# Optimization experiments

Hardware: AMD Instinct MI355X
Metric: run time of the kernel (lower is better)

The kernel has to match this reference:

```python
import jax, jax.numpy as jnp
import numpy as np

H, N_EMB, D_EMB, D_UP = 1024, 8192, 512, 2048
B, T, BB, M, K_LABELS = 4, 4096, 512, 4096, 64


def _rms(x, w, eps=1e-6):
    xf = x.astype(jnp.float32)
    var = jnp.mean(xf * xf, axis=-1, keepdims=True)
    return (w * (xf * jax.lax.rsqrt(var + eps))).astype(x.dtype)


def setup_inputs() -> dict:
    key = jax.random.key(0)
    ks = jax.random.split(key, 8)
    bt = B * T
    inp = jax.random.normal(ks[0], (B, T, H), jnp.float32)
    w_k = jax.random.normal(ks[1], (N_EMB, H), jnp.float32) * 0.02
    w_v = jax.random.normal(ks[2], (N_EMB, D_EMB), jnp.float32) * 0.02
    w_up = jax.random.normal(ks[3], (D_UP, D_EMB), jnp.float32) * 0.02
    w_mix = jax.random.normal(ks[4], (H, D_UP + H), jnp.float32) * 0.02
    fw = jax.random.permutation(ks[5], bt)
    bw = jnp.argsort(fw)  # inverse permutation
    seq_sort = jax.random.randint(ks[6], (bt,), 0, K_LABELS)
    keep_cols = jnp.arange(M)  # keep first M of N_EMB rows
    emb_alloc = jnp.arange(N_EMB) % K_LABELS  # every label present among kept rows
    starts = jnp.zeros((bt,), jnp.int32)
    ends = jnp.full((bt,), M, jnp.int32)
    return {
        'input': inp, 'fw': fw, 'bw': bw, 'seq_sort': seq_sort,
        'keep_cols': keep_cols, 'emb_alloc': emb_alloc,
        'starts': starts, 'ends': ends, 'bb': BB,
        'w_k_weight': w_k, 'w_v_weight': w_v, 'w_up_weight': w_up,
        'w_mix_weight': w_mix,
        'norm_in_weight': jnp.ones((H,), jnp.float32),
        'norm_out_weight': jnp.ones((D_UP,), jnp.float32),
    }


def reference(input, fw, bw, seq_sort, keep_cols, emb_alloc, starts, ends, bb,
              w_k_weight, w_v_weight, w_up_weight, w_mix_weight,
              norm_in_weight, norm_out_weight):
    b, t, h = input.shape
    A = _rms(input, norm_in_weight)                      # [b,t,h]
    Bm = w_k_weight[keep_cols]                           # [m,h]
    Cm = w_v_weight[keep_cols]                           # [m,d_emb]
    la = emb_alloc[keep_cols]                            # [m]
    A = A.reshape(-1, h)[fw].reshape(-1, bb, h)          # [nb,bb,h]
    ss = seq_sort.reshape(-1, bb)                        # [nb,bb]
    st = starts.reshape(-1, bb).min(axis=-1)             # [nb]
    en = ends.reshape(-1, bb).max(axis=-1)               # [nb]
    # ragged per-block slice B[start:end] expressed as a kv range mask,
    # combined with the equality mask seq_sort[q] == emb_alloc[kv]
    scores = jnp.einsum('nqh,kh->nqk', A, Bm)            # [nb,bb,m]
    kv = jnp.arange(Bm.shape[0])
    mask = ((ss[:, :, None] == la[None, None, :])
            & (kv[None, None, :] >= st[:, None, None])
            & (kv[None, None, :] < en[:, None, None]))
    scores = jnp.where(mask, scores, -jnp.inf)
    p = jax.nn.softmax(scores, axis=-1)
    comb = jnp.einsum('nqk,kd->nqd', p, Cm)              # [nb,bb,d_emb]
    d_emb = Cm.shape[-1]
    comb = comb.reshape(-1, d_emb)[bw].reshape(b, t, d_emb)
    up = comb @ w_up_weight.T                            # [b,t,d_up]
    cat = jnp.concatenate([_rms(up, norm_out_weight), input], axis=-1)
    return cat @ w_mix_weight.T                          # [b,t,h]
```

## Files before the change

### kernel.cpp

```cpp
#include <hip/hip_runtime.h>
#include <hip/hip_bf16.h>
#include <cstdint>
#include <cstddef>

#define Hh 1024
#define D_EMB 512
#define D_UP 2048
#define BT 16384
#define BB_ 512
#define Mm 4096
#define MmP 4160
#define NB 32
#define KL 64
#define NXCD 8

typedef __attribute__((ext_vector_type(4))) float f4;
typedef __attribute__((ext_vector_type(4))) __bf16 bf4;
typedef __attribute__((ext_vector_type(8))) __bf16 bf8;
typedef __attribute__((ext_vector_type(4))) float f32x4;

__device__ __forceinline__ void gl_lds16(const void* g, void* l) {
  __builtin_amdgcn_global_load_lds((__attribute__((address_space(1))) void*)g,
                                   (__attribute__((address_space(3))) void*)l, 16, 0, 0);
}

__global__ __launch_bounds__(256) void conv_bf16_kernel(const float* __restrict__ src,
                                                        __bf16* __restrict__ dst, int n4) {
  int i = blockIdx.x * 256 + threadIdx.x;
  if (i >= n4) return;
  f4 v = ((const f4*)src)[i];
  bf4 o = {(__bf16)v[0], (__bf16)v[1], (__bf16)v[2], (__bf16)v[3]};
  ((bf4*)dst)[i] = o;
}

__global__ __launch_bounds__(256) void gather_bf16_kernel(const float* __restrict__ src,
                                                          const int* __restrict__ idx,
                                                          __bf16* __restrict__ dst, int cols4) {
  int row = blockIdx.x;
  const f4* s = (const f4*)src + (size_t)idx[row] * cols4;
  bf4* d = (bf4*)dst + (size_t)row * cols4;
  for (int i = threadIdx.x; i < cols4; i += 256) {
    f4 v = s[i];
    bf4 o = {(__bf16)v[0], (__bf16)v[1], (__bf16)v[2], (__bf16)v[3]};
    d[i] = o;
  }
}

__global__ __launch_bounds__(256) void la_kernel(const int* __restrict__ keep,
                                                 const int* __restrict__ emb,
                                                 int* __restrict__ la, int m) {
  int i = blockIdx.x * 256 + threadIdx.x;
  if (i < m) la[i] = emb[keep[i]];
}

__global__ __launch_bounds__(256) void range_kernel(const int* __restrict__ starts,
                                                    const int* __restrict__ ends,
                                                    int* __restrict__ stA, int* __restrict__ enA) {
  int n = blockIdx.x;
  int t = threadIdx.x, lane = t & 63, wv = t >> 6;
  int s1 = min(starts[n * BB_ + t], starts[n * BB_ + t + 256]);
  int e1 = max(ends[n * BB_ + t], ends[n * BB_ + t + 256]);
#pragma unroll
  for (int off = 32; off; off >>= 1) {
    s1 = min(s1, __shfl_xor(s1, off));
    e1 = max(e1, __shfl_xor(e1, off));
  }
  __shared__ int ssh[4], esh[4];
  if (lane == 0) { ssh[wv] = s1; esh[wv] = e1; }
  __syncthreads();
  if (t == 0) {
    int s = ssh[0], e = esh[0];
#pragma unroll
    for (int k = 1; k < 4; ++k) { s = min(s, ssh[k]); e = max(e, esh[k]); }
    stA[n] = s; enA[n] = e;
  }
}

__global__ __launch_bounds__(256) void hist_kernel(const int* __restrict__ la,
                                                   int* __restrict__ goff) {
  __shared__ int cnt[KL];
  int tid = threadIdx.x;
  if (tid < KL) cnt[tid] = 0;
  __syncthreads();
  for (int k = tid; k < Mm; k += 256) atomicAdd(&cnt[la[k]], 1);
  __syncthreads();
  if (tid == 0) {
    int a = 0;
    for (int s = 0; s < KL; ++s) { goff[s] = a; a += cnt[s]; }
    goff[KL] = a;
  }
}

__global__ __launch_bounds__(256) void place_kernel(const int* __restrict__ la,
                                                    const int* __restrict__ keep,
                                                    const int* __restrict__ goff,
                                                    int* __restrict__ gk,
                                                    int* __restrict__ ridx) {
  int s = blockIdx.x;
  int tid = threadIdx.x, lane = tid & 63, wv = tid >> 6;
  __shared__ int wc[4];
  __shared__ int run;
  if (tid == 0) run = goff[s];
  __syncthreads();
  for (int base = 0; base < Mm; base += 256) {
    int k = base + tid;
    bool f = (la[k] == s);
    unsigned long long msk = __ballot(f);
    int myidx = __popcll(msk & ((1ull << lane) - 1ull));
    if (lane == 0) wc[wv] = __popcll(msk);
    __syncthreads();
    int woff = 0, tot = 0;
#pragma unroll
    for (int w = 0; w < 4; ++w) {
      if (w < wv) woff += wc[w];
      tot += wc[w];
    }
    int rbase = run;
    if (f) {
      int p = rbase + woff + myidx;
      gk[p] = k;
      ridx[p] = keep[k];
    }
    __syncthreads();
    if (tid == 0) run = rbase + tot;
    __syncthreads();
  }
}

__global__ __launch_bounds__(256) void lohi_kernel(const int* __restrict__ gk,
                                                   const int* __restrict__ goff,
                                                   const int* __restrict__ stA,
                                                   const int* __restrict__ enA,
                                                   int* __restrict__ loA, int* __restrict__ hiA) {
  int i = blockIdx.x * 256 + threadIdx.x;
  if (i >= NB * KL) return;
  int n = i / KL, s = i % KL;
  int b = goff[s], e = goff[s + 1];
  int st = stA[n], en = enA[n];
  int lo = b, hi = e;
  while (lo < hi) { int mid = (lo + hi) >> 1; if (gk[mid] < st) lo = mid + 1; else hi = mid; }
  int L = lo;
  lo = b; hi = e;
  while (lo < hi) { int mid = (lo + hi) >> 1; if (gk[mid] < en) lo = mid + 1; else hi = mid; }
  loA[i] = L;
  hiA[i] = lo;
}

__global__ __launch_bounds__(256) void vt_kernel(const float* __restrict__ wv_,
                                                 const int* __restrict__ ridx,
                                                 __bf16* __restrict__ VT) {
  int pb = blockIdx.x * 64;
  int db = blockIdx.y * 64;
  __shared__ float T[64][65];
  int t = threadIdx.x;
  int dl = t & 63, g = t >> 6;
  for (int i = g * 16; i < g * 16 + 16; ++i) {
    int r = ridx[pb + i];
    T[dl][i] = wv_[(size_t)r * D_EMB + db + dl];
  }
  __syncthreads();
  int pl = t & 63;
  for (int j = g * 16; j < g * 16 + 16; ++j) {
    VT[(size_t)(db + j) * MmP + pb + pl] = (__bf16)T[j][pl];
  }
}

__global__ __launch_bounds__(256) void qsort_kernel(const int* __restrict__ seq_sort,
                                                    int* __restrict__ qidx,
                                                    int* __restrict__ qoffA,
                                                    int* __restrict__ qcntA) {
  int n = blockIdx.x, tid = threadIdx.x;
  __shared__ int cnt[KL], pos[KL], pref[KL];
  if (tid < KL) cnt[tid] = 0;
  __syncthreads();
  int s0 = seq_sort[n * BB_ + tid];
  int s1 = seq_sort[n * BB_ + tid + 256];
  atomicAdd(&cnt[s0], 1);
  atomicAdd(&cnt[s1], 1);
  __syncthreads();
  if (tid == 0) {
    int a = 0;
    for (int s = 0; s < KL; ++s) { pref[s] = a; a += cnt[s]; }
  }
  __syncthreads();
  if (tid < KL) {
    pos[tid] = pref[tid];
    qoffA[n * KL + tid] = pref[tid];
    qcntA[n * KL + tid] = cnt[tid];
  }
  __syncthreads();
  int p0 = atomicAdd(&pos[s0], 1);
  qidx[n * BB_ + p0] = n * BB_ + tid;
  int p1 = atomicAdd(&pos[s1], 1);
  qidx[n * BB_ + p1] = n * BB_ + tid + 256;
}

__global__ __launch_bounds__(256) void rms_in_kernel(const float* __restrict__ input,
                                                     const int* __restrict__ fw,
                                                     const float* __restrict__ wn,
                                                     __bf16* __restrict__ Aperm,
                                                     __bf16* __restrict__ inb) {
  int wv = threadIdx.x >> 6, lane = threadIdx.x & 63;
  int j = blockIdx.x * 4 + wv;
  {
    const f4* src = (const f4*)(input + (size_t)fw[j] * Hh);
    f4 v[4];
    float ss = 0.f;
#pragma unroll
    for (int c = 0; c < 4; ++c) {
      v[c] = src[c * 64 + lane];
      ss += v[c][0] * v[c][0] + v[c][1] * v[c][1] + v[c][2] * v[c][2] + v[c][3] * v[c][3];
    }
#pragma unroll
    for (int off = 32; off; off >>= 1) ss += __shfl_xor(ss, off);
    float sc = rsqrtf(ss * (1.f / Hh) + 1e-6f);
    const f4* w4 = (const f4*)wn;
    bf4* dst = (bf4*)(Aperm + (size_t)j * Hh);
#pragma unroll
    for (int c = 0; c < 4; ++c) {
      f4 w = w4[c * 64 + lane];
      bf4 o = {(__bf16)(v[c][0] * sc * w[0]), (__bf16)(v[c][1] * sc * w[1]),
               (__bf16)(v[c][2] * sc * w[2]), (__bf16)(v[c][3] * sc * w[3])};
      dst[c * 64 + lane] = o;
    }
  }
  {
    const f4* src = (const f4*)(input + (size_t)j * Hh);
    bf4* dst = (bf4*)(inb + (size_t)j * Hh);
#pragma unroll
    for (int c = 0; c < 4; ++c) {
      f4 t = src[c * 64 + lane];
      bf4 o = {(__bf16)t[0], (__bf16)t[1], (__bf16)t[2], (__bf16)t[3]};
      dst[c * 64 + lane] = o;
    }
  }
}

__global__ __launch_bounds__(256) void attn3_kernel(const __bf16* __restrict__ Aperm,
                                                    const __bf16* __restrict__ Ks,
                                                    const __bf16* __restrict__ VT,
                                                    const int* __restrict__ qidx,
                                                    const int* __restrict__ qoffA,
                                                    const int* __restrict__ qcntA,
                                                    const int* __restrict__ loA,
                                                    const int* __restrict__ hiA,
                                                    const int* __restrict__ fw,
                                                    __bf16* __restrict__ comb) {
  int g = blockIdx.x;
  int qcnt = qcntA[g];
  if (qcnt == 0) return;
  int n = g >> 6;
  int qbase = n * BB_ + qoffA[g];
  int lo = loA[g], hi = hiA[g];
  if (lo >= hi) return;
  int tid = threadIdx.x, lane = tid & 63, wv = tid >> 6;
  int c = lane & 15, rg = lane >> 4;
  __shared__ float Sbuf[16][66];
  __shared__ __align__(16) __bf16 Plds[16][72];
  __shared__ float scl[16], lrec[16];

  for (int qt = 0; qt < qcnt; qt += 16) {
    int ql = qt + c;
    int j = qidx[qbase + (ql < qcnt ? ql : 0)];
    const __bf16* arow = Aperm + (size_t)j * Hh + rg * 8;

    float m[4] = {-1e30f, -1e30f, -1e30f, -1e30f};
    float l[4] = {0.f, 0.f, 0.f, 0.f};
    f32x4 acc[8];
    f32x4 zero = {0.f, 0.f, 0.f, 0.f};
#pragma unroll
    for (int t8 = 0; t8 < 8; ++t8) acc[t8] = zero;

    for (int p0 = lo; p0 < hi; p0 += 64) {
      int kvcol = p0 + wv * 16 + c;
      const __bf16* brow = Ks + (size_t)kvcol * Hh + rg * 8;
      f32x4 sacc = zero;
#pragma unroll
      for (int ks = 0; ks < 32; ++ks) {
        bf8 af = *(const bf8*)(arow + ks * 32);
        bf8 bf_ = *(const bf8*)(brow + ks * 32);
        sacc = __builtin_amdgcn_mfma_f32_16x16x32_bf16(af, bf_, sacc, 0, 0, 0);
      }
      bool valid = kvcol < hi;
#pragma unroll
      for (int r = 0; r < 4; ++r) Sbuf[rg * 4 + r][wv * 16 + c] = valid ? sacc[r] : -1e30f;
      __syncthreads();

#pragma unroll
      for (int r = 0; r < 4; ++r) {
        int q = wv * 4 + r;
        float s = Sbuf[q][lane];
        float cm = s;
#pragma unroll
        for (int off = 32; off; off >>= 1) cm = fmaxf(cm, __shfl_xor(cm, off));
        float mn = fmaxf(m[r], cm);
        float sc = __expf(m[r] - mn);
        float pv = __expf(s - mn);
        float ssum = pv;
#pragma unroll
        for (int off = 32; off; off >>= 1) ssum += __shfl_xor(ssum, off);
        l[r] = l[r] * sc + ssum;
        m[r] = mn;
        Plds[q][lane] = (__bf16)pv;
        if (lane == 0) scl[q] = sc;
      }
      __syncthreads();

      float sf[4];
#pragma unroll
      for (int r = 0; r < 4; ++r) sf[r] = scl[rg * 4 + r];
#pragma unroll
      for (int t8 = 0; t8 < 8; ++t8)
#pragma unroll
        for (int r = 0; r < 4; ++r) acc[t8][r] *= sf[r];

      bf8 pa0 = *(const bf8*)(&Plds[c][rg * 8]);
      bf8 pa1 = *(const bf8*)(&Plds[c][32 + rg * 8]);
#pragma unroll
      for (int tt = 0; tt < 8; ++tt) {
        int d = wv * 128 + tt * 16 + c;
        const __bf16* vrow = VT + (size_t)d * MmP + p0 + rg * 8;
        bf8 b0 = *(const bf8*)(vrow);
        bf8 b1 = *(const bf8*)(vrow + 32);
        acc[tt] = __builtin_amdgcn_mfma_f32_16x16x32_bf16(pa0, b0, acc[tt], 0, 0, 0);
        acc[tt] = __builtin_amdgcn_mfma_f32_16x16x32_bf16(pa1, b1, acc[tt], 0, 0, 0);
      }
      __syncthreads();
    }

    if (lane == 0) {
#pragma unroll
      for (int r = 0; r < 4; ++r) lrec[wv * 4 + r] = l[r];
    }
    __syncthreads();
    float inv[4];
    size_t obase[4];
    bool oval[4];
#pragma unroll
    for (int r = 0; r < 4; ++r) {
      int qq = qt + rg * 4 + r;
      oval[r] = qq < qcnt;
      int j2 = qidx[qbase + (oval[r] ? qq : 0)];
      obase[r] = (size_t)fw[j2] * D_EMB;
      float lv = lrec[rg * 4 + r];
      inv[r] = 1.f / lv;
    }
#pragma unroll
    for (int tt = 0; tt < 8; ++tt) {
      int d = wv * 128 + tt * 16 + c;
#pragma unroll
      for (int r = 0; r < 4; ++r) {
        if (oval[r]) comb[obase[r] + d] = (__bf16)(acc[tt][r] * inv[r]);
      }
    }
    __syncthreads();
  }
}

template <bool OUT_BF16>
__global__ __launch_bounds__(512, 2) void gemm8p(const __bf16* __restrict__ x0, int k0,
                                                 const __bf16* __restrict__ x1, int k1,
                                                 const __bf16* __restrict__ w,
                                                 void* __restrict__ outp, int Mt, int Nt) {
  __shared__ __align__(16) __bf16 lds[4][2][256 * 32];
  const int nwg = Mt * Nt;
  const int bid = blockIdx.x;
  const int swz = (bid % NXCD) * (nwg / NXCD) + bid / NXCD;
  const int m0 = (swz / Nt) * 256, n0 = (swz % Nt) * 256;
  const int K = k0 + k1;
  const int NT = K >> 5;
  const int N = Nt * 256;
  const int tid = threadIdx.x, lane = tid & 63, wvi = tid >> 6;
  const int wr = wvi >> 2, wc = wvi & 3;

  const int srow = tid >> 2;
  const int spb = (tid & 3) * 16;

  const int c = lane & 15, rg = lane >> 4;
  const int fa_off = c * 64 + ((rg ^ ((c >> 1) & 3)) << 4);

  auto stage_half = [&](int t, int j) {
    int kg = t * 32;
    const __bf16* xs;
    int ld, kk;
    if (kg < k0) { xs = x0; ld = k0; kk = kg; }
    else         { xs = x1; ld = k1; kk = kg - k0; }
    int b = t & 3;
    int r = j * 128 + srow;
    int lcol = (spb ^ (((r >> 1) & 3) << 4)) >> 1;
    gl_lds16(xs + (size_t)(m0 + r) * ld + kk + lcol,
             (void*)((char*)&lds[b][0][0] + r * 64 + spb));
    gl_lds16(w + (size_t)(n0 + r) * K + kg + lcol,
             (void*)((char*)&lds[b][1][0] + r * 64 + spb));
  };

  f32x4 acc[8][4];
  f32x4 zero = {0.f, 0.f, 0.f, 0.f};
#pragma unroll
  for (int a = 0; a < 8; ++a)
#pragma unroll
    for (int bnx = 0; bnx < 4; ++bnx) acc[a][bnx] = zero;

#pragma unroll
  for (int t = 0; t < 3; ++t) {
    stage_half(t, 0);
    stage_half(t, 1);
  }
  asm volatile("s_waitcnt vmcnt(8)" ::: "memory");
  __builtin_amdgcn_s_barrier();

  for (int t = 0; t < NT; ++t) {
    const char* Abase = (const char*)&lds[t & 3][0][0];
    const char* Bbase = (const char*)&lds[t & 3][1][0];
    bf8 bfr[4];
#pragma unroll
    for (int ri = 0; ri < 2; ++ri) {
      if (t + 3 < NT) stage_half(t + 3, ri);
      bf8 afr[4];
#pragma unroll
      for (int fi = 0; fi < 4; ++fi)
        afr[fi] = *(const bf8*)(Abase + (wr * 128 + ri * 64 + fi * 16) * 64 + fa_off);
      if (ri == 0) {
#pragma unroll
        for (int fi = 0; fi < 4; ++fi)
          bfr[fi] = *(const bf8*)(Bbase + (wc * 64 + fi * 16) * 64 + fa_off);
      }
      __builtin_amdgcn_s_barrier();
      __builtin_amdgcn_s_setprio(1);
#pragma unroll
      for (int fi = 0; fi < 4; ++fi)
#pragma unroll
        for (int ni = 0; ni < 4; ++ni)
          acc[ri * 4 + fi][ni] =
              __builtin_amdgcn_mfma_f32_16x16x32_bf16(afr[fi], bfr[ni], acc[ri * 4 + fi][ni], 0, 0, 0);
      __builtin_amdgcn_s_setprio(0);
      if (ri == 1) asm volatile("s_waitcnt vmcnt(8)" ::: "memory");
      __builtin_amdgcn_s_barrier();
    }
  }

  const int r0 = (lane >> 4) * 4, cc = lane & 15;
#pragma unroll
  for (int mi = 0; mi < 8; ++mi) {
    int rowb = m0 + wr * 128 + (mi >> 2) * 64 + (mi & 3) * 16 + r0;
#pragma unroll
    for (int ni = 0; ni < 4; ++ni) {
      int col = n0 + wc * 64 + ni * 16 + cc;
#pragma unroll
      for (int r = 0; r < 4; ++r) {
        float v = acc[mi][ni][r];
        if (OUT_BF16)
          ((__bf16*)outp)[(size_t)(rowb + r) * N + col] = (__bf16)v;
        else
          ((float*)outp)[(size_t)(rowb + r) * N + col] = v;
      }
    }
  }
}

__global__ __launch_bounds__(256) void rms_up_kernel(__bf16* __restrict__ up,
                                                     const float* __restrict__ wn) {
  int wv = threadIdx.x >> 6, lane = threadIdx.x & 63;
  size_t j = (size_t)blockIdx.x * 4 + wv;
  bf8* row = (bf8*)(up + j * D_UP);
  bf8 v[4];
  float ss = 0.f;
#pragma unroll
  for (int c = 0; c < 4; ++c) {
    v[c] = row[c * 64 + lane];
#pragma unroll
    for (int i = 0; i < 8; ++i) { float f = (float)v[c][i]; ss += f * f; }
  }
#pragma unroll
  for (int off = 32; off; off >>= 1) ss += __shfl_xor(ss, off);
  float sc = rsqrtf(ss * (1.f / D_UP) + 1e-6f);
#pragma unroll
  for (int c = 0; c < 4; ++c) {
    int ebase = (c * 64 + lane) * 8;
    f4 wa = *(const f4*)(wn + ebase);
    f4 wb = *(const f4*)(wn + ebase + 4);
    bf8 o;
#pragma unroll
    for (int i = 0; i < 4; ++i) o[i] = (__bf16)((float)v[c][i] * sc * wa[i]);
#pragma unroll
    for (int i = 0; i < 4; ++i) o[4 + i] = (__bf16)((float)v[c][4 + i] * sc * wb[i]);
    row[c * 64 + lane] = o;
  }
}

extern "C" void kernel_launch(void* const* d_in, const int* in_sizes, int n_in, void* d_out,
                              int out_size, void* d_ws, size_t ws_size, hipStream_t stream) {
  const float* input = (const float*)d_in[0];
  const int* fw = (const int*)d_in[1];
  const int* seq_sort = (const int*)d_in[3];
  const int* keep_cols = (const int*)d_in[4];
  const int* emb_alloc = (const int*)d_in[5];
  const int* starts = (const int*)d_in[6];
  const int* ends = (const int*)d_in[7];
  const float* w_k = (const float*)d_in[9];
  const float* w_v = (const float*)d_in[10];
  const float* w_up = (const float*)d_in[11];
  const float* w_mix = (const float*)d_in[12];
  const float* w_nin = (const float*)d_in[13];
  const float* w_nout = (const float*)d_in[14];

  char* p = (char*)d_ws;
  auto take = [&](size_t b) {
    void* r = (void*)p;
    p += (b + 255) & ~(size_t)255;
    return r;
  };
  __bf16* Aperm = (__bf16*)take((size_t)BT * Hh * 2);
  __bf16* inb = (__bf16*)take((size_t)BT * Hh * 2);
  __bf16* comb = (__bf16*)take((size_t)BT * D_EMB * 2);
  __bf16* up = (__bf16*)take((size_t)BT * D_UP * 2);
  __bf16* Ks = (__bf16*)take((size_t)MmP * Hh * 2);
  __bf16* VT = (__bf16*)take((size_t)D_EMB * MmP * 2);
  __bf16* wupB = (__bf16*)take((size_t)D_UP * D_EMB * 2);
  __bf16* wmixB = (__bf16*)take((size_t)Hh * (D_UP + Hh) * 2);
  int* la = (int*)take(Mm * 4);
  int* stA = (int*)take(NB * 4);
  int* enA = (int*)take(NB * 4);
  int* goff = (int*)take((KL + 1) * 4);
  int* gk = (int*)take(Mm * 4);
  int* ridx = (int*)take(Mm * 4);
  int* loA = (int*)take(NB * KL * 4);
  int* hiA = (int*)take(NB * KL * 4);
  int* qidx = (int*)take(BT * 4);
  int* qoffA = (int*)take(NB * KL * 4);
  int* qcntA = (int*)take(NB * KL * 4);

  conv_bf16_kernel<<<(D_UP * D_EMB / 4 + 255) / 256, 256, 0, stream>>>(w_up, wupB, D_UP * D_EMB / 4);
  conv_bf16_kernel<<<(Hh * (D_UP + Hh) / 4 + 255) / 256, 256, 0, stream>>>(w_mix, wmixB,
                                                                           Hh * (D_UP + Hh) / 4);
  la_kernel<<<Mm / 256, 256, 0, stream>>>(keep_cols, emb_alloc, la, Mm);
  range_kernel<<<NB, 256, 0, stream>>>(starts, ends, stA, enA);
  hist_kernel<<<1, 256, 0, stream>>>(la, goff);
  place_kernel<<<KL, 256, 0, stream>>>(la, keep_cols, goff, gk, ridx);
  lohi_kernel<<<(NB * KL + 255) / 256, 256, 0, stream>>>(gk, goff, stA, enA, loA, hiA);
  gather_bf16_kernel<<<Mm, 256, 0, stream>>>(w_k, ridx, Ks, Hh / 4);
  vt_kernel<<<dim3(Mm / 64, D_EMB / 64), 256, 0, stream>>>(w_v, ridx, VT);
  qsort_kernel<<<NB, 256, 0, stream>>>(seq_sort, qidx, qoffA, qcntA);

  rms_in_kernel<<<BT / 4, 256, 0, stream>>>(input, fw, w_nin, Aperm, inb);
  attn3_kernel<<<NB * KL, 256, 0, stream>>>(Aperm, Ks, VT, qidx, qoffA, qcntA, loA, hiA, fw, comb);
  gemm8p<true><<<BT / 256 * (D_UP / 256), 512, 0, stream>>>(comb, D_EMB, (const __bf16*)nullptr, 0,
                                                            wupB, (void*)up, BT / 256, D_UP / 256);
  rms_up_kernel<<<BT / 4, 256, 0, stream>>>(up, w_nout);
  gemm8p<false><<<BT / 256 * (Hh / 256), 512, 0, stream>>>(up, D_UP, inb, Hh, wmixB, d_out,
                                                           BT / 256, Hh / 256);
}
```

Measured before the change: 332.9 us.

## Restructure attention to one wave per group with register-resident softmax

The attention kernel now gives each wave its own (block,label) group instead of one workgroup per group. Each wave computes a 16x64 score tile with four MFMA chains, does the online softmax in registers via lane shuffles, and keeps all 512 output dims in 32 accumulators. This removes the LDS score/P buffers and three __syncthreads per kv tile, and stages output through LDS for coalesced 16-byte stores. The RMS-in kernel now reads input rows contiguously once and scatters Aperm through the inverse permutation. VT padding columns are zero-filled so the pad region is defined. The cost is heavy register use: 128 accumulator floats per lane, with launch bounds of 2 workgroups per CU. Load balance across waves may also be uneven because label groups differ in size.

```diff
diff --git a/kernel.cpp b/kernel.cpp
--- a/kernel.cpp
+++ b/kernel.cpp
@@ -155,8 +155,13 @@
   int t = threadIdx.x;
   int dl = t & 63, g = t >> 6;
   for (int i = g * 16; i < g * 16 + 16; ++i) {
-    int r = ridx[pb + i];
-    T[dl][i] = wv_[(size_t)r * D_EMB + db + dl];
+    int pos = pb + i;
+    float val = 0.f;
+    if (pos < Mm) {
+      int r = ridx[pos];
+      val = wv_[(size_t)r * D_EMB + db + dl];
+    }
+    T[dl][i] = val;
   }
   __syncthreads();
   int pl = t & 63;
@@ -196,164 +201,165 @@
 }
 
 __global__ __launch_bounds__(256) void rms_in_kernel(const float* __restrict__ input,
-                                                     const int* __restrict__ fw,
+                                                     const int* __restrict__ bw,
                                                      const float* __restrict__ wn,
                                                      __bf16* __restrict__ Aperm,
                                                      __bf16* __restrict__ inb) {
   int wv = threadIdx.x >> 6, lane = threadIdx.x & 63;
   int j = blockIdx.x * 4 + wv;
-  {
-    const f4* src = (const f4*)(input + (size_t)fw[j] * Hh);
-    f4 v[4];
-    float ss = 0.f;
-#pragma unroll
-    for (int c = 0; c < 4; ++c) {
-      v[c] = src[c * 64 + lane];
-      ss += v[c][0] * v[c][0] + v[c][1] * v[c][1] + v[c][2] * v[c][2] + v[c][3] * v[c][3];
-    }
-#pragma unroll
-    for (int off = 32; off; off >>= 1) ss += __shfl_xor(ss, off);
-    float sc = rsqrtf(ss * (1.f / Hh) + 1e-6f);
-    const f4* w4 = (const f4*)wn;
-    bf4* dst = (bf4*)(Aperm + (size_t)j * Hh);
-#pragma unroll
-    for (int c = 0; c < 4; ++c) {
-      f4 w = w4[c * 64 + lane];
-      bf4 o = {(__bf16)(v[c][0] * sc * w[0]), (__bf16)(v[c][1] * sc * w[1]),
-               (__bf16)(v[c][2] * sc * w[2]), (__bf16)(v[c][3] * sc * w[3])};
-      dst[c * 64 + lane] = o;
-    }
-  }
-  {
-    const f4* src = (const f4*)(input + (size_t)j * Hh);
-    bf4* dst = (bf4*)(inb + (size_t)j * Hh);
-#pragma unroll
-    for (int c = 0; c < 4; ++c) {
-      f4 t = src[c * 64 + lane];
-      bf4 o = {(__bf16)t[0], (__bf16)t[1], (__bf16)t[2], (__bf16)t[3]};
-      dst[c * 64 + lane] = o;
-    }
-  }
-}
-
-__global__ __launch_bounds__(256) void attn3_kernel(const __bf16* __restrict__ Aperm,
-                                                    const __bf16* __restrict__ Ks,
-                                                    const __bf16* __restrict__ VT,
-                                                    const int* __restrict__ qidx,
-                                                    const int* __restrict__ qoffA,
-                                                    const int* __restrict__ qcntA,
-                                                    const int* __restrict__ loA,
-                                                    const int* __restrict__ hiA,
-                                                    const int* __restrict__ fw,
-                                                    __bf16* __restrict__ comb) {
-  int g = blockIdx.x;
+  const f4* src = (const f4*)(input + (size_t)j * Hh);
+  f4 v[4];
+  float ss = 0.f;
+#pragma unroll
+  for (int c = 0; c < 4; ++c) {
+    v[c] = src[c * 64 + lane];
+    ss += v[c][0] * v[c][0] + v[c][1] * v[c][1] + v[c][2] * v[c][2] + v[c][3] * v[c][3];
+  }
+#pragma unroll
+  for (int off = 32; off; off >>= 1) ss += __shfl_xor(ss, off);
+  float sc = rsqrtf(ss * (1.f / Hh) + 1e-6f);
+  bf4* dstI = (bf4*)(inb + (size_t)j * Hh);
+#pragma unroll
+  for (int c = 0; c < 4; ++c) {
+    bf4 o = {(__bf16)v[c][0], (__bf16)v[c][1], (__bf16)v[c][2], (__bf16)v[c][3]};
+    dstI[c * 64 + lane] = o;
+  }
+  int dj = bw[j];
+  const f4* w4 = (const f4*)wn;
+  bf4* dstA = (bf4*)(Aperm + (size_t)dj * Hh);
+#pragma unroll
+  for (int c = 0; c < 4; ++c) {
+    f4 w = w4[c * 64 + lane];
+    bf4 o = {(__bf16)(v[c][0] * sc * w[0]), (__bf16)(v[c][1] * sc * w[1]),
+             (__bf16)(v[c][2] * sc * w[2]), (__bf16)(v[c][3] * sc * w[3])};
+    dstA[c * 64 + lane] = o;
+  }
+}
+
+__global__ __launch_bounds__(256, 2) void attn4_kernel(const __bf16* __restrict__ Aperm,
+                                                       const __bf16* __restrict__ Ks,
+                                                       const __bf16* __restrict__ VT,
+                                                       const int* __restrict__ qidx,
+                                                       const int* __restrict__ qoffA,
+                                                       const int* __restrict__ qcntA,
+                                                       const int* __restrict__ loA,
+                                                       const int* __restrict__ hiA,
+                                                       const int* __restrict__ fw,
+                                                       __bf16* __restrict__ comb) {
+  __shared__ __align__(16) __bf16 owb[4][16][528];
+  int wv = threadIdx.x >> 6, lane = threadIdx.x & 63;
+  int g = blockIdx.x * 4 + wv;
   int qcnt = qcntA[g];
-  if (qcnt == 0) return;
+  int lo = loA[g], hi = hiA[g];
+  if (qcnt == 0 || lo >= hi) return;
   int n = g >> 6;
   int qbase = n * BB_ + qoffA[g];
-  int lo = loA[g], hi = hiA[g];
-  if (lo >= hi) return;
-  int tid = threadIdx.x, lane = tid & 63, wv = tid >> 6;
   int c = lane & 15, rg = lane >> 4;
-  __shared__ float Sbuf[16][66];
-  __shared__ __align__(16) __bf16 Plds[16][72];
-  __shared__ float scl[16], lrec[16];
+  int sl_a = c + ((rg & 1) << 5);
+  int sl_b = sl_a + 16;
+  bool hiKt = (rg & 2) != 0;
+  const __bf16* vbase = VT + (size_t)c * MmP + rg * 8;
 
   for (int qt = 0; qt < qcnt; qt += 16) {
     int ql = qt + c;
-    int j = qidx[qbase + (ql < qcnt ? ql : 0)];
-    const __bf16* arow = Aperm + (size_t)j * Hh + rg * 8;
-
-    float m[4] = {-1e30f, -1e30f, -1e30f, -1e30f};
-    float l[4] = {0.f, 0.f, 0.f, 0.f};
-    f32x4 acc[8];
+    int j = qidx[qbase + (ql < qcnt ? ql : qcnt - 1)];
+    const __bf16* qrow = Aperm + (size_t)j * Hh + rg * 8;
+
+    float m = -1e30f, lsum = 0.f;
+    f32x4 acc[32];
     f32x4 zero = {0.f, 0.f, 0.f, 0.f};
 #pragma unroll
-    for (int t8 = 0; t8 < 8; ++t8) acc[t8] = zero;
+    for (int ff = 0; ff < 32; ++ff) acc[ff] = zero;
 
     for (int p0 = lo; p0 < hi; p0 += 64) {
-      int kvcol = p0 + wv * 16 + c;
-      const __bf16* brow = Ks + (size_t)kvcol * Hh + rg * 8;
-      f32x4 sacc = zero;
+      const __bf16* kb = Ks + (size_t)(p0 + c) * Hh + rg * 8;
+      f32x4 sN[4];
+#pragma unroll
+      for (int kt = 0; kt < 4; ++kt) sN[kt] = zero;
 #pragma unroll
       for (int ks = 0; ks < 32; ++ks) {
-        bf8 af = *(const bf8*)(arow + ks * 32);
-        bf8 bf_ = *(const bf8*)(brow + ks * 32);
-        sacc = __builtin_amdgcn_mfma_f32_16x16x32_bf16(af, bf_, sacc, 0, 0, 0);
+        bf8 qf = *(const bf8*)(qrow + ks * 32);
+#pragma unroll
+        for (int kt = 0; kt < 4; ++kt) {
+          bf8 kf = *(const bf8*)(kb + (size_t)kt * 16 * Hh + ks * 32);
+          sN[kt] = __builtin_amdgcn_mfma_f32_16x16x32_bf16(kf, qf, sN[kt], 0, 0, 0);
+        }
       }
-      bool valid = kvcol < hi;
-#pragma unroll
-      for (int r = 0; r < 4; ++r) Sbuf[rg * 4 + r][wv * 16 + c] = valid ? sacc[r] : -1e30f;
-      __syncthreads();
-
-#pragma unroll
-      for (int r = 0; r < 4; ++r) {
-        int q = wv * 4 + r;
-        float s = Sbuf[q][lane];
-        float cm = s;
-#pragma unroll
-        for (int off = 32; off; off >>= 1) cm = fmaxf(cm, __shfl_xor(cm, off));
-        float mn = fmaxf(m[r], cm);
-        float sc = __expf(m[r] - mn);
-        float pv = __expf(s - mn);
-        float ssum = pv;
-#pragma unroll
-        for (int off = 32; off; off >>= 1) ssum += __shfl_xor(ssum, off);
-        l[r] = l[r] * sc + ssum;
-        m[r] = mn;
-        Plds[q][lane] = (__bf16)pv;
-        if (lane == 0) scl[q] = sc;
+      float smax = -1e30f;
+#pragma unroll
+      for (int kt = 0; kt < 4; ++kt)
+#pragma unroll
+        for (int r = 0; r < 4; ++r) {
+          int kv = p0 + kt * 16 + rg * 4 + r;
+          float sv = (kv < hi) ? sN[kt][r] : -1e30f;
+          sN[kt][r] = sv;
+          smax = fmaxf(smax, sv);
+        }
+      smax = fmaxf(smax, __shfl_xor(smax, 16));
+      smax = fmaxf(smax, __shfl_xor(smax, 32));
+      float mn = fmaxf(m, smax);
+      float sc = __expf(m - mn);
+      float sum = 0.f;
+#pragma unroll
+      for (int kt = 0; kt < 4; ++kt)
+#pragma unroll
+        for (int r = 0; r < 4; ++r) {
+          float pv = __expf(sN[kt][r] - mn);
+          sN[kt][r] = pv;
+          sum += pv;
+        }
+      sum += __shfl_xor(sum, 16);
+      sum += __shfl_xor(sum, 32);
+      lsum = lsum * sc + sum;
+      m = mn;
+#pragma unroll
+      for (int ff = 0; ff < 32; ++ff) acc[ff] = acc[ff] * sc;
+
+      bf8 pbh[2];
+#pragma unroll
+      for (int h = 0; h < 2; ++h) {
+        float e[8];
+#pragma unroll
+        for (int r = 0; r < 4; ++r) {
+          float a0 = __shfl(sN[2 * h][r], sl_a);
+          float a1 = __shfl(sN[2 * h + 1][r], sl_a);
+          e[r] = hiKt ? a1 : a0;
+          float b0 = __shfl(sN[2 * h][r], sl_b);
+          float b1 = __shfl(sN[2 * h + 1][r], sl_b);
+          e[4 + r] = hiKt ? b1 : b0;
+        }
+        bf8 pb;
+#pragma unroll
+        for (int i = 0; i < 8; ++i) pb[i] = (__bf16)e[i];
+        pbh[h] = pb;
       }
-      __syncthreads();
-
-      float sf[4];
-#pragma unroll
-      for (int r = 0; r < 4; ++r) sf[r] = scl[rg * 4 + r];
-#pragma unroll
-      for (int t8 = 0; t8 < 8; ++t8)
-#pragma unroll
-        for (int r = 0; r < 4; ++r) acc[t8][r] *= sf[r];
-
-      bf8 pa0 = *(const bf8*)(&Plds[c][rg * 8]);
-      bf8 pa1 = *(const bf8*)(&Plds[c][32 + rg * 8]);
-#pragma unroll
-      for (int tt = 0; tt < 8; ++tt) {
-        int d = wv * 128 + tt * 16 + c;
-        const __bf16* vrow = VT + (size_t)d * MmP + p0 + rg * 8;
-        bf8 b0 = *(const bf8*)(vrow);
-        bf8 b1 = *(const bf8*)(vrow + 32);
-        acc[tt] = __builtin_amdgcn_mfma_f32_16x16x32_bf16(pa0, b0, acc[tt], 0, 0, 0);
-        acc[tt] = __builtin_amdgcn_mfma_f32_16x16x32_bf16(pa1, b1, acc[tt], 0, 0, 0);
+#pragma unroll
+      for (int ff = 0; ff < 32; ++ff) {
+        const __bf16* vr = vbase + (size_t)ff * (16 * MmP) + p0;
+        bf8 v0 = *(const bf8*)(vr);
+        bf8 v1 = *(const bf8*)(vr + 32);
+        acc[ff] = __builtin_amdgcn_mfma_f32_16x16x32_bf16(v0, pbh[0], acc[ff], 0, 0, 0);
+        acc[ff] = __builtin_amdgcn_mfma_f32_16x16x32_bf16(v1, pbh[1], acc[ff], 0, 0, 0);
       }
-      __syncthreads();
-    }
-
-    if (lane == 0) {
-#pragma unroll
-      for (int r = 0; r < 4; ++r) lrec[wv * 4 + r] = l[r];
-    }
-    __syncthreads();
-    float inv[4];
-    size_t obase[4];
-    bool oval[4];
-#pragma unroll
-    for (int r = 0; r < 4; ++r) {
-      int qq = qt + rg * 4 + r;
-      oval[r] = qq < qcnt;
-      int j2 = qidx[qbase + (oval[r] ? qq : 0)];
-      obase[r] = (size_t)fw[j2] * D_EMB;
-      float lv = lrec[rg * 4 + r];
-      inv[r] = 1.f / lv;
-    }
-#pragma unroll
-    for (int tt = 0; tt < 8; ++tt) {
-      int d = wv * 128 + tt * 16 + c;
-#pragma unroll
-      for (int r = 0; r < 4; ++r) {
-        if (oval[r]) comb[obase[r] + d] = (__bf16)(acc[tt][r] * inv[r]);
-      }
-    }
-    __syncthreads();
+    }
+
+    float inv = 1.f / lsum;
+#pragma unroll
+    for (int ff = 0; ff < 32; ++ff) {
+      bf4 o;
+#pragma unroll
+      for (int r = 0; r < 4; ++r) o[r] = (__bf16)(acc[ff][r] * inv);
+      *(bf4*)&owb[wv][c][ff * 16 + rg * 4] = o;
+    }
+    int qp = qt + (lane >> 2);
+    bool vq = qp < qcnt;
+    size_t ob = 0;
+    if (vq) ob = (size_t)fw[qidx[qbase + qp]] * D_EMB + (lane & 3) * 8;
+#pragma unroll
+    for (int it = 0; it < 16; ++it) {
+      bf8 o = *(const bf8*)&owb[wv][lane >> 2][(lane & 3) * 8 + it * 32];
+      if (vq) *(bf8*)(comb + ob + (size_t)it * 32) = o;
+    }
   }
 }
 
@@ -492,6 +498,7 @@
                               int out_size, void* d_ws, size_t ws_size, hipStream_t stream) {
   const float* input = (const float*)d_in[0];
   const int* fw = (const int*)d_in[1];
+  const int* bw = (const int*)d_in[2];
   const int* seq_sort = (const int*)d_in[3];
   const int* keep_cols = (const int*)d_in[4];
   const int* emb_alloc = (const int*)d_in[5];
@@ -539,11 +546,12 @@
   place_kernel<<<KL, 256, 0, stream>>>(la, keep_cols, goff, gk, ridx);
   lohi_kernel<<<(NB * KL + 255) / 256, 256, 0, stream>>>(gk, goff, stA, enA, loA, hiA);
   gather_bf16_kernel<<<Mm, 256, 0, stream>>>(w_k, ridx, Ks, Hh / 4);
-  vt_kernel<<<dim3(Mm / 64, D_EMB / 64), 256, 0, stream>>>(w_v, ridx, VT);
+  vt_kernel<<<dim3(MmP / 64, D_EMB / 64), 256, 0, stream>>>(w_v, ridx, VT);
   qsort_kernel<<<NB, 256, 0, stream>>>(seq_sort, qidx, qoffA, qcntA);
 
-  rms_in_kernel<<<BT / 4, 256, 0, stream>>>(input, fw, w_nin, Aperm, inb);
-  attn3_kernel<<<NB * KL, 256, 0, stream>>>(Aperm, Ks, VT, qidx, qoffA, qcntA, loA, hiA, fw, comb);
+  rms_in_kernel<<<BT / 4, 256, 0, stream>>>(input, bw, w_nin, Aperm, inb);
+  attn4_kernel<<<NB * KL / 4, 256, 0, stream>>>(Aperm, Ks, VT, qidx, qoffA, qcntA, loA, hiA, fw,
+                                                comb);
   gemm8p<true><<<BT / 256 * (D_UP / 256), 512, 0, stream>>>(comb, D_EMB, (const __bf16*)nullptr, 0,
                                                             wupB, (void*)up, BT / 256, D_UP / 256);
   rms_up_kernel<<<BT / 4, 256, 0, stream>>>(up, w_nout);
```

Result: slower. 360.8 us (+8.4%).
